# Kernel optimization log

Hardware: AMD Instinct MI355X
Metric: run time of the kernel (lower is better)

## Reference

```python
import jax, jax.numpy as jnp
import numpy as np

B, S, H, G, W_LOC = 2, 4096, 12, 64, 513  # Longformer-base: window=2*256+1, 64 global slots


def setup_inputs() -> dict:
    key = jax.random.key(0)
    k1, = jax.random.split(key, 1)
    attention_probs = jax.random.uniform(k1, (B, S, H, G + W_LOC), dtype=jnp.float32)
    attention_mask = jnp.zeros((B, S), dtype=jnp.float32)  # all tokens currently kept
    # global tokens are the first G positions of every batch; nonzero(as_tuple) index arrays
    b_idx = jnp.repeat(jnp.arange(B, dtype=jnp.int64), G)
    g_idx = jnp.tile(jnp.arange(G, dtype=jnp.int64), B)
    return {
        "attention_mask": attention_mask,
        "attention_probs": attention_probs,
        "keep_threshold": jnp.asarray(0.005, dtype=jnp.float32),  # base 0.01*6/12 + learned 0
        "max_num_global_attn_indices": G,
        "loc_b": b_idx, "loc_i": g_idx,
        "glob_b": b_idx, "glob_i": g_idx,
    }


def reference(attention_mask, attention_probs, keep_threshold,
              max_num_global_attn_indices, loc_b, loc_i, glob_b, glob_i):
    Gn = max_num_global_attn_indices
    b, s, h, wg = attention_probs.shape
    w = wg - Gn  # local window size, odd
    half = w // 2

    # zero out rows of already-masked tokens (attention_mask < 0)
    probs = jnp.where((attention_mask < 0)[:, :, None, None], 0.0, attention_probs)

    gl = probs[..., :Gn]                              # [B,S,H,G]
    lo = jnp.transpose(probs[..., Gn:], (0, 2, 1, 3))  # [B,H,S,W]

    # anti-diagonal (key-column) sums of the local band; equals the source's
    # conv2d-with-flipped-identity + slice: out[j] = sum_c lo[j + half - c, c]
    lo_p = jnp.pad(lo, ((0, 0), (0, 0), (half, half), (0, 0)))  # [B,H,S+W-1,W]
    rows = jnp.arange(s)[:, None] + (w - 1) - jnp.arange(w)[None, :]  # [S,W]
    diag = lo_p[:, :, rows, jnp.arange(w)[None, :]]  # [B,H,S,W]
    local_sum = diag.sum(axis=(1, 3))                # [B,S] (summed over heads too)

    global_sum = gl.sum(axis=(1, 2))                 # [B,G]
    probs_sum = local_sum.at[loc_b, loc_i].add(global_sum[glob_b, glob_i])

    probs_max = probs_sum.max(axis=-1, keepdims=True)
    scores = probs_sum / probs_max

    thr = jnp.maximum(jnp.float32(1e-5), jnp.asarray(keep_threshold, jnp.float32).reshape(()))
    new_attention_mask = jnp.where(scores < thr, jnp.float32(-10000.0), jnp.float32(0.0))
    return new_attention_mask, scores
```

## Files before the change

kernel.cpp:

```cpp
#include <hip/hip_runtime.h>
#include <float.h>

#define Bsz 2
#define Ssz 4096
#define Hsz 12
#define Gsz 64
#define Wsz 513
#define Csz (Gsz + Wsz)
#define ROW (Hsz * Csz)
#define HALF 256
#define RPB 8
#define WIN (RPB + Wsz - 1)

#define PSUM_SZ ((size_t)Bsz * Ssz)
#define GACC_SZ ((size_t)Bsz * Gsz)

__global__ __launch_bounds__(256) void k1_fused(
    const float* __restrict__ probs, const float* __restrict__ mask,
    float* __restrict__ psum, float* __restrict__ gacc)
{
    __shared__ float win[WIN];
    const int t = threadIdx.x;
    const int row0 = blockIdx.x * RPB;
    const int b = row0 / Ssz;

    for (int w = t; w < WIN; w += 256) win[w] = 0.f;
    __syncthreads();

    float scale[RPB];
    #pragma unroll
    for (int r = 0; r < RPB; ++r)
        scale[r] = (mask[row0 + r] < 0.f) ? 0.f : 1.f;

    const float* base = probs + (size_t)row0 * ROW;
    float g = 0.f;

    for (int c = t; c < Csz; c += 256) {
        #pragma unroll
        for (int r = 0; r < RPB; ++r) {
            float v = 0.f;
            #pragma unroll
            for (int h = 0; h < Hsz; ++h)
                v += base[(size_t)r * ROW + h * Csz + c];
            v *= scale[r];
            if (c < Gsz) g += v;
            else atomicAdd(&win[r + (c - Gsz)], v);
        }
    }
    __syncthreads();

    const int i_base = (row0 - b * Ssz) - HALF;
    for (int w = t; w < WIN; w += 256) {
        const int i = i_base + w;
        if (i >= 0 && i < Ssz) atomicAdd(&psum[b * Ssz + i], win[w]);
    }
    if (t < Gsz) atomicAdd(&gacc[b * Gsz + t], g);
}

__global__ __launch_bounds__(1024) void k4_final(
    const float* __restrict__ psum, const float* __restrict__ gacc,
    const float* __restrict__ thr_p,
    const int* __restrict__ loc_b, const int* __restrict__ loc_i,
    const int* __restrict__ glob_b, const int* __restrict__ glob_i,
    int n_idx, float* __restrict__ out)
{
    __shared__ float p_lds[Ssz];
    __shared__ float red[16];
    const int b = blockIdx.x;
    const int t = threadIdx.x;
    const float* p = psum + (size_t)b * Ssz;

    for (int i = t; i < Ssz; i += 1024) p_lds[i] = p[i];
    __syncthreads();

    if (t < n_idx && loc_b[t] == b)
        atomicAdd(&p_lds[loc_i[t]], gacc[glob_b[t] * Gsz + glob_i[t]]);
    __syncthreads();

    float m = -FLT_MAX;
    for (int i = t; i < Ssz; i += 1024) m = fmaxf(m, p_lds[i]);
    #pragma unroll
    for (int off = 32; off >= 1; off >>= 1) m = fmaxf(m, __shfl_down(m, off, 64));

    const int wave = t >> 6, lane = t & 63;
    if (lane == 0) red[wave] = m;
    __syncthreads();
    if (t == 0) {
        float mm = red[0];
        #pragma unroll
        for (int w = 1; w < 16; ++w) mm = fmaxf(mm, red[w]);
        red[0] = mm;
    }
    __syncthreads();
    const float mx = red[0];
    const float thr = fmaxf(1e-5f, thr_p[0]);

    for (int i = t; i < Ssz; i += 1024) {
        float sc = p_lds[i] / mx;
        out[(size_t)Bsz * Ssz + (size_t)b * Ssz + i] = sc;
        out[(size_t)b * Ssz + i] = (sc < thr) ? -10000.f : 0.f;
    }
}

extern "C" void kernel_launch(void* const* d_in, const int* in_sizes, int n_in,
                              void* d_out, int out_size, void* d_ws, size_t ws_size,
                              hipStream_t stream)
{
    const float* mask  = (const float*)d_in[0];
    const float* probs = (const float*)d_in[1];
    const float* thr   = (const float*)d_in[2];
    const int* loc_b  = (const int*)d_in[4];
    const int* loc_i  = (const int*)d_in[5];
    const int* glob_b = (const int*)d_in[6];
    const int* glob_i = (const int*)d_in[7];
    const int n_idx = in_sizes[4];

    float* psum = (float*)d_ws;
    float* gacc = psum + PSUM_SZ;
    float* out  = (float*)d_out;

    hipMemsetAsync(psum, 0, (PSUM_SZ + GACC_SZ) * sizeof(float), stream);

    k1_fused<<<dim3(Bsz * Ssz / RPB), dim3(256), 0, stream>>>(probs, mask, psum, gacc);
    k4_final<<<dim3(Bsz), dim3(1024), 0, stream>>>(psum, gacc, thr,
                                                   loc_b, loc_i, glob_b, glob_i,
                                                   n_idx, out);
}
```

Before: 340.6 us.

## Stream probs as float4 with per-element LDS atomics into swizzled slots

Replaces the per-column head-summing loop, which issued strided scalar loads, with a flat float4 stream over each block's contiguous 8-row slab. Every element is atomically added into a shared slot array that covers both global and local columns, and the slot index is swizzled to spread LDS bank conflicts. The goal is fully coalesced wide global loads, at the price of one LDS atomic per element instead of one per (row, column). Column and row indices are tracked incrementally, stepping by 1024 elements per iteration.

```diff
diff --git a/kernel.cpp b/kernel.cpp
--- a/kernel.cpp
+++ b/kernel.cpp
@@ -10,51 +10,60 @@
 #define ROW (Hsz * Csz)
 #define HALF 256
 #define RPB 8
-#define WIN (RPB + Wsz - 1)
+#define NSLOT (Gsz + RPB - 1 + Wsz)
+#define NF4 (RPB * ROW / 4)
 
 #define PSUM_SZ ((size_t)Bsz * Ssz)
 #define GACC_SZ ((size_t)Bsz * Gsz)
+
+__device__ __forceinline__ int SWZ(int s) { return ((s & 3) * 146) + (s >> 2); }
 
 __global__ __launch_bounds__(256) void k1_fused(
     const float* __restrict__ probs, const float* __restrict__ mask,
     float* __restrict__ psum, float* __restrict__ gacc)
 {
-    __shared__ float win[WIN];
+    __shared__ float U[NSLOT];
+    __shared__ float scl[RPB + 1];
     const int t = threadIdx.x;
     const int row0 = blockIdx.x * RPB;
     const int b = row0 / Ssz;
 
-    for (int w = t; w < WIN; w += 256) win[w] = 0.f;
+    for (int u = t; u < NSLOT; u += 256) U[u] = 0.f;
+    if (t < RPB) scl[t] = (mask[row0 + t] < 0.f) ? 0.f : 1.f;
+    if (t == RPB) scl[RPB] = 0.f;
     __syncthreads();
 
-    float scale[RPB];
-    #pragma unroll
-    for (int r = 0; r < RPB; ++r)
-        scale[r] = (mask[row0 + r] < 0.f) ? 0.f : 1.f;
+    const float4* __restrict__ src = (const float4*)(probs + (size_t)row0 * ROW);
+    int c = 4 * t; if (c >= Csz) c -= Csz;
+    int rowpos = 4 * t;
+    int r = 0;
+    float sc = scl[0];
 
-    const float* base = probs + (size_t)row0 * ROW;
-    float g = 0.f;
-
-    for (int c = t; c < Csz; c += 256) {
+    for (int fi = t; fi < NF4; fi += 256) {
+        float4 v = src[fi];
+        float vv[4] = {v.x, v.y, v.z, v.w};
         #pragma unroll
-        for (int r = 0; r < RPB; ++r) {
-            float v = 0.f;
-            #pragma unroll
-            for (int h = 0; h < Hsz; ++h)
-                v += base[(size_t)r * ROW + h * Csz + c];
-            v *= scale[r];
-            if (c < Gsz) g += v;
-            else atomicAdd(&win[r + (c - Gsz)], v);
+        for (int j = 0; j < 4; ++j) {
+            int cj = c + j; if (cj >= Csz) cj -= Csz;
+            int slot = (cj < Gsz) ? cj : cj + r;
+            atomicAdd(&U[SWZ(slot)], vv[j] * sc);
         }
+        c += 447; if (c >= Csz) c -= Csz;
+        rowpos += 1024;
+        if (rowpos >= ROW) { rowpos -= ROW; ++r; sc = scl[r]; }
     }
     __syncthreads();
 
-    const int i_base = (row0 - b * Ssz) - HALF;
-    for (int w = t; w < WIN; w += 256) {
-        const int i = i_base + w;
-        if (i >= 0 && i < Ssz) atomicAdd(&psum[b * Ssz + i], win[w]);
+    const int s0 = row0 - b * Ssz;
+    for (int slot = t; slot < NSLOT; slot += 256) {
+        float val = U[SWZ(slot)];
+        if (slot < Gsz) {
+            atomicAdd(&gacc[b * Gsz + slot], val);
+        } else {
+            int i = s0 + slot - (Gsz + HALF);
+            if (i >= 0 && i < Ssz) atomicAdd(&psum[b * Ssz + i], val);
+        }
     }
-    if (t < Gsz) atomicAdd(&gacc[b * Gsz + t], g);
 }
 
 __global__ __launch_bounds__(1024) void k4_final(
```

Result: slower. 525.8 us (+54.4%).
